# Optimization experiments

Hardware: AMD Instinct MI355X
Metric: run time of the kernel (lower is better)

The kernel has to match this reference:

```python
import jax, jax.numpy as jnp
import numpy as np

N, E, B = 60000, 360000, 64        # nodes, edges, graphs
IN_DIM, HID, L, NCLS = 256, 512, 3, 1000
EPS = 1e-5                          # BatchNorm1d eps


def setup_inputs() -> dict:
    key = jax.random.key(0)
    ks = jax.random.split(key, 10)
    s = 0.05
    x = jax.random.normal(ks[0], (N, IN_DIM), dtype=jnp.float32)
    edge_index = jax.random.randint(ks[1], (2, E), 0, N, dtype=jnp.int32)
    batch = jnp.sort(jax.random.randint(ks[2], (N,), 0, B, dtype=jnp.int32))
    W_embed = jax.random.normal(ks[3], (IN_DIM, HID), dtype=jnp.float32) * s
    # per-block params (all 3 blocks have identical shapes -> stacked on axis 0)
    W1 = jax.random.normal(ks[4], (L, 2 * HID, HID), dtype=jnp.float32) * s
    b1 = jnp.zeros((L, HID), jnp.float32)
    g1 = jnp.ones((L, HID), jnp.float32)
    be1 = jnp.zeros((L, HID), jnp.float32)
    W2 = jax.random.normal(ks[5], (L, 2 * HID, HID), dtype=jnp.float32) * s
    b2 = jnp.zeros((L, HID), jnp.float32)
    g2 = jnp.ones((L, HID), jnp.float32)
    be2 = jnp.zeros((L, HID), jnp.float32)
    W_att = jax.random.normal(ks[6], (HID, 1), dtype=jnp.float32) * s
    W_read = jax.random.normal(ks[7], (HID, NCLS), dtype=jnp.float32) * s
    return dict(x=x, edge_index=edge_index, batch=batch, W_embed=W_embed,
                W1=W1, b1=b1, g1=g1, be1=be1, W2=W2, b2=b2, g2=g2, be2=be2,
                W_att=W_att, W_read=W_read)


def _segment_mean(vals, idx, num):
    s = jax.ops.segment_sum(vals, idx, num_segments=num)
    c = jax.ops.segment_sum(jnp.ones((vals.shape[0], 1), vals.dtype), idx, num_segments=num)
    return s / jnp.maximum(c, 1.0)


def _bn(h, g, b):  # BatchNorm1d, training-mode batch statistics (biased var)
    m = h.mean(0)
    v = jnp.mean((h - m) ** 2, axis=0)
    return (h - m) * jax.lax.rsqrt(v + EPS) * g + b


def _sage(h, src, dst, W, b):
    # MySAGEConv (position=False -> message = x_j), aggr='mean', concat=True, L2 normalize
    aggr = _segment_mean(h[src], dst, h.shape[0])          # [N, d] mean of neighbor msgs
    out = jnp.concatenate([h, aggr], axis=-1) @ W + b      # [N, 2d] @ [2d, d]
    norm = jnp.linalg.norm(out, axis=-1, keepdims=True)
    return out / jnp.maximum(norm, 1e-12)                  # F.normalize(p=2)


def reference(x, edge_index, batch, W_embed, W1, b1, g1, be1,
              W2, b2, g2, be2, W_att, W_read):
    src, dst = edge_index[0], edge_index[1]
    h = x @ W_embed
    for l in range(L):  # MySAGEConvBlock, gcn_num=2, has_linear_in_block=False
        identity = h
        out = jax.nn.relu(_bn(_sage(h, src, dst, W1[l], b1[l]), g1[l], be1[l]))
        out = jax.nn.relu(_bn(_sage(out, src, dst, W2[l], b2[l]), g2[l], be2[l]))
        h = out + identity  # residual (dims match)
    # AttentionClass
    att = jax.nn.sigmoid(h @ W_att)           # [N, 1]
    hx = (att * h + h) * 0.5
    hg = _segment_mean(hx, batch, B)          # global mean pool per graph
    return hg @ W_read                        # [B, 1000] logits
```

## Files before the change

### kernel.cpp

```cpp
#include <hip/hip_runtime.h>
#include <math.h>

#define N_NODES 60000
#define N_EDGES 360000
#define N_GRAPH 64
#define HID 512
#define NCLS 1000
#define BN_EPS 1e-5f
#define NS ((size_t)N_NODES * HID)
#define NB 235
#define STRIPS 469

typedef __bf16 bf16x8 __attribute__((ext_vector_type(8)));
typedef float f32x4 __attribute__((ext_vector_type(4)));

static __device__ __forceinline__ unsigned short f2bf(float f) {
  unsigned u = __float_as_uint(f);
  unsigned r = (u + 0x7fffu + ((u >> 16) & 1u)) >> 16;
  return (unsigned short)r;
}
static __device__ __forceinline__ float bfLo(unsigned u) { return __uint_as_float(u << 16); }
static __device__ __forceinline__ float bfHi(unsigned u) { return __uint_as_float(u & 0xffff0000u); }
static __device__ __forceinline__ unsigned packbf(float a, float b) {
  return (unsigned)f2bf(a) | ((unsigned)f2bf(b) << 16);
}

__global__ void write_sentinel(float* out, float v) { out[0] = v; }

__global__ __launch_bounds__(256) void cvt_bf16(const float* __restrict__ X,
                                                unsigned short* __restrict__ Y,
                                                long n4) {
  long i = (long)blockIdx.x * 256 + threadIdx.x;
  if (i >= n4) return;
  float4 f = *(const float4*)(X + i * 4);
  uint2 o;
  o.x = packbf(f.x, f.y);
  o.y = packbf(f.z, f.w);
  *(uint2*)(Y + i * 4) = o;
}

__global__ __launch_bounds__(256) void wtrans(const float* __restrict__ W,
                                              unsigned short* __restrict__ Wt,
                                              int K, int N) {
  __shared__ float sh[32][33];
  int kt = blockIdx.x * 32, nt = blockIdx.y * 32;
  int tx = threadIdx.x & 31, ty = threadIdx.x >> 5;
#pragma unroll
  for (int i = 0; i < 4; ++i)
    sh[ty + i * 8][tx] = W[(size_t)(kt + ty + i * 8) * N + nt + tx];
  __syncthreads();
#pragma unroll
  for (int i = 0; i < 4; ++i)
    Wt[(size_t)(nt + ty + i * 8) * K + kt + tx] = f2bf(sh[tx][ty + i * 8]);
}

__global__ __launch_bounds__(256) void count_deg(const int* __restrict__ dst,
                                                 int* __restrict__ deg, int E) {
  int e = blockIdx.x * 256 + threadIdx.x;
  if (e < E) atomicAdd(&deg[dst[e]], 1);
}

__global__ __launch_bounds__(256) void make_invdeg(const int* __restrict__ deg,
                                                   float* __restrict__ inv, int n) {
  int i = blockIdx.x * 256 + threadIdx.x;
  if (i < n) inv[i] = 1.0f / fmaxf((float)deg[i], 1.0f);
}

__global__ __launch_bounds__(256) void scan_part(const int* __restrict__ deg,
                                                 int* __restrict__ bsum, int n) {
  __shared__ int sh[256];
  int i = blockIdx.x * 256 + threadIdx.x;
  sh[threadIdx.x] = (i < n) ? deg[i] : 0;
  __syncthreads();
  for (int off = 128; off; off >>= 1) {
    if (threadIdx.x < off) sh[threadIdx.x] += sh[threadIdx.x + off];
    __syncthreads();
  }
  if (threadIdx.x == 0) bsum[blockIdx.x] = sh[0];
}

__global__ __launch_bounds__(256) void scan_bsums(int* __restrict__ bsum, int nb) {
  __shared__ int sh[256];
  int t = threadIdx.x;
  int v = (t < nb) ? bsum[t] : 0;
  sh[t] = v;
  __syncthreads();
  for (int off = 1; off < 256; off <<= 1) {
    int u = (t >= off) ? sh[t - off] : 0;
    __syncthreads();
    sh[t] += u;
    __syncthreads();
  }
  if (t < nb) bsum[t] = sh[t] - v;
}

__global__ __launch_bounds__(256) void scan_final(const int* __restrict__ deg,
                                                  const int* __restrict__ bsum,
                                                  int* __restrict__ rowptr, int n) {
  __shared__ int sh[256];
  int t = threadIdx.x;
  int i = blockIdx.x * 256 + t;
  int v = (i < n) ? deg[i] : 0;
  sh[t] = v;
  __syncthreads();
  for (int off = 1; off < 256; off <<= 1) {
    int u = (t >= off) ? sh[t - off] : 0;
    __syncthreads();
    sh[t] += u;
    __syncthreads();
  }
  if (i < n) rowptr[i + 1] = bsum[blockIdx.x] + sh[t];
  if (i == 0) rowptr[0] = 0;
}

__global__ __launch_bounds__(256) void fill_csr(const int* __restrict__ src,
                                                const int* __restrict__ dst,
                                                const int* __restrict__ rowptr,
                                                int* __restrict__ fillc,
                                                int* __restrict__ esrc, int E) {
  int e = blockIdx.x * 256 + threadIdx.x;
  if (e < E) {
    int d = dst[e];
    int pos = rowptr[d] + atomicAdd(&fillc[d], 1);
    esrc[pos] = src[e];
  }
}

__global__ __launch_bounds__(256) void bcount(const int* __restrict__ batch,
                                              float* __restrict__ bcnt, int n) {
  __shared__ int h[N_GRAPH];
  if (threadIdx.x < N_GRAPH) h[threadIdx.x] = 0;
  __syncthreads();
  int i = blockIdx.x * 256 + threadIdx.x;
  if (i < n) atomicAdd(&h[batch[i]], 1);
  __syncthreads();
  if (threadIdx.x < N_GRAPH && h[threadIdx.x])
    atomicAdd(&bcnt[threadIdx.x], (float)h[threadIdx.x]);
}

#define GEMM_BODY(Xb, ldx, Wtb, ldw, bias_p, outp, KDIM)                        \
  const int wv = tid >> 6, lane = tid & 63;                                     \
  const int wm = (wv >> 1) * 64, wn = (wv & 1) * 64;                            \
  const int lm = lane & 15, quad = lane >> 4;                                   \
  const int grow = lane & 15, gseg = (lane >> 4) * 8;                           \
  f32x4 zero; zero[0] = 0.f; zero[1] = 0.f; zero[2] = 0.f; zero[3] = 0.f;       \
  f32x4 acc[4][4];                                                              \
  _Pragma("unroll") for (int i = 0; i < 4; ++i)                                 \
    _Pragma("unroll") for (int j = 0; j < 4; ++j) acc[i][j] = zero;             \
  for (int kt = 0; kt < (KDIM); kt += 32) {                                     \
    __syncthreads();                                                            \
    _Pragma("unroll") for (int r = 0; r < 2; ++r) {                             \
      int chunk = wv + r * 4;                                                   \
      int row = chunk * 16 + grow;                                              \
      const unsigned short* ga = (Xb) + (size_t)(bm + row) * (ldx) + kt + gseg; \
      const unsigned short* gb = (Wtb) + (size_t)(bn + row) * (ldw) + kt + gseg;\
      __builtin_amdgcn_global_load_lds(                                         \
          (const __attribute__((address_space(1))) unsigned int*)ga,            \
          (__attribute__((address_space(3))) unsigned int*)(As + chunk * 512),  \
          16, 0, 0);                                                            \
      __builtin_amdgcn_global_load_lds(                                         \
          (const __attribute__((address_space(1))) unsigned int*)gb,            \
          (__attribute__((address_space(3))) unsigned int*)(Bs + chunk * 512),  \
          16, 0, 0);                                                            \
    }                                                                           \
    __syncthreads();                                                            \
    bf16x8 af[4], bfr[4];                                                       \
    _Pragma("unroll") for (int i = 0; i < 4; ++i)                               \
      af[i] = *(const bf16x8*)(As + (wm / 16 + i) * 512 + lane * 8);            \
    _Pragma("unroll") for (int j = 0; j < 4; ++j)                               \
      bfr[j] = *(const bf16x8*)(Bs + (wn / 16 + j) * 512 + lane * 8);           \
    _Pragma("unroll") for (int i = 0; i < 4; ++i)                               \
      _Pragma("unroll") for (int j = 0; j < 4; ++j)                             \
        acc[i][j] = __builtin_amdgcn_mfma_f32_16x16x32_bf16(af[i], bfr[j],      \
                                                            acc[i][j], 0, 0, 0);\
  }                                                                             \
  const int qr = quad * 4;                                                      \
  const int rl = tid >> 4, seg = (tid & 15) * 8;                                \
  _Pragma("unroll") for (int p = 0; p < 2; ++p) {                               \
    __syncthreads();                                                            \
    if ((wv >> 1) == p) {                                                       \
      _Pragma("unroll") for (int j = 0; j < 4; ++j) {                           \
        int col = wn + j * 16 + lm;                                             \
        float bvv = (bias_p) ? (bias_p)[bn + col] : 0.f;                        \
        _Pragma("unroll") for (int i = 0; i < 4; ++i)                           \
          _Pragma("unroll") for (int r = 0; r < 4; ++r)                         \
            Cs[i * 16 + qr + r][col] = f2bf(acc[i][j][r] + bvv);                \
      }                                                                         \
    }                                                                           \
    __syncthreads();                                                            \
    _Pragma("unroll") for (int pass = 0; pass < 4; ++pass) {                    \
      int row = bm + p * 64 + pass * 16 + rl;                                   \
      if (row < M)                                                              \
        *(uint4*)((outp) + (size_t)row * 512 + bn + seg) =                      \
            *(const uint4*)(&Cs[pass * 16 + rl][seg]);                          \
    }                                                                           \
  }

__global__ __launch_bounds__(256) void gemm_glds(
    const unsigned short* __restrict__ Xb, int ldx, int K,
    const unsigned short* __restrict__ Wt, int ldw,
    const float* __restrict__ bias,
    unsigned short* __restrict__ outB, int M) {
  __shared__ __align__(16) unsigned short As[128 * 32];
  __shared__ __align__(16) unsigned short Bs[128 * 32];
  __shared__ __align__(16) unsigned short Cs[64][136];
  const int tid = threadIdx.x;
  const int L = blockIdx.x;
  const int xcd = L & 7, li = L >> 3;
  const int strip = xcd * 59 + (li >> 2);
  if (strip >= STRIPS) return;
  const int bm = strip * 128;
  const int bn = (li & 3) * 128;
  GEMM_BODY(Xb, ldx, Wt, ldw, bias, outB, K)
}

__global__ __launch_bounds__(256) void gemm_dual(
    const unsigned short* __restrict__ Xb, int ldx,
    const unsigned short* __restrict__ Wt,
    const float* __restrict__ biasA,
    unsigned short* __restrict__ outA, unsigned short* __restrict__ outBf,
    int M) {
  __shared__ __align__(16) unsigned short As[128 * 32];
  __shared__ __align__(16) unsigned short Bs[128 * 32];
  __shared__ __align__(16) unsigned short Cs[64][136];
  const int tid = threadIdx.x;
  const int L = blockIdx.x;
  const int xcd = L & 7, li = L >> 3;
  const int strip = xcd * 59 + (li >> 3);
  if (strip >= STRIPS) return;
  const int cb = li & 7;
  const int bm = strip * 128;
  const int bn = (cb & 3) * 128;
  const unsigned short* Wtb = Wt + (cb < 4 ? 0 : 512);
  const float* bias = (cb < 4) ? biasA : nullptr;
  unsigned short* outp = (cb < 4) ? outA : outBf;
  GEMM_BODY(Xb, ldx, Wtb, 1024, bias, outp, 512)
}

__global__ __launch_bounds__(512) void gemm_strip(
    const unsigned short* __restrict__ Xb, int ldx,
    const unsigned short* __restrict__ Wt, int ldw,
    const float* __restrict__ bias,
    unsigned short* __restrict__ outB, int M) {
  __shared__ __align__(16) unsigned short As[64][40];
  const int tid = threadIdx.x;
  const int bm = blockIdx.x * 64;
  const int wv = tid >> 6, lane = tid & 63;
  const int lm = lane & 15, quad = lane >> 4, lk = quad * 8;
  const int cb = wv * 64;
  const int arow = tid >> 3, aseg = (tid & 7) * 4;

  f32x4 zero;
  zero[0] = 0.f; zero[1] = 0.f; zero[2] = 0.f; zero[3] = 0.f;
  f32x4 acc[4][4];
#pragma unroll
  for (int i = 0; i < 4; ++i)
#pragma unroll
    for (int j = 0; j < 4; ++j) acc[i][j] = zero;

  for (int kt = 0; kt < 512; kt += 32) {
    uint2 av = make_uint2(0, 0);
    int gr = bm + arow;
    if (gr < M) av = *(const uint2*)(Xb + (size_t)gr * ldx + kt + aseg);
    bf16x8 bfr[4];
#pragma unroll
    for (int j = 0; j < 4; ++j)
      bfr[j] = *(const bf16x8*)(Wt + (size_t)(cb + j * 16 + lm) * ldw + kt + lk);
    __syncthreads();
    *(uint2*)(&As[arow][aseg]) = av;
    __syncthreads();
    bf16x8 af[4];
#pragma unroll
    for (int i = 0; i < 4; ++i) af[i] = *(const bf16x8*)(&As[i * 16 + lm][lk]);
#pragma unroll
    for (int i = 0; i < 4; ++i)
#pragma unroll
      for (int j = 0; j < 4; ++j)
        acc[i][j] = __builtin_amdgcn_mfma_f32_16x16x32_bf16(af[i], bfr[j], acc[i][j], 0, 0, 0);
  }

  const int qr = quad * 4;
#pragma unroll
  for (int j = 0; j < 4; ++j) {
    int col = cb + j * 16 + lm;
    float bvv = bias ? bias[col] : 0.f;
#pragma unroll
    for (int i = 0; i < 4; ++i) {
      int rbase = bm + i * 16 + qr;
#pragma unroll
      for (int r = 0; r < 4; ++r) {
        int row = rbase + r;
        if (row < M) outB[(size_t)row * 512 + col] = f2bf(acc[i][j][r] + bvv);
      }
    }
  }
}

__global__ __launch_bounds__(256) void aggr_norm(
    unsigned short* __restrict__ Ya, const unsigned short* __restrict__ Yb,
    const int* __restrict__ rowptr, const int* __restrict__ esrc,
    const float* __restrict__ invdeg, int M) {
  int d = blockIdx.x * 4 + (threadIdx.x >> 6);
  int lane = threadIdx.x & 63;
  if (d >= M) return;
  float acc[8] = {0.f, 0.f, 0.f, 0.f, 0.f, 0.f, 0.f, 0.f};
  int beg = rowptr[d], end = rowptr[d + 1];
  for (int e = beg; e < end; ++e) {
    int s = esrc[e];
    uint4 u = *(const uint4*)(Yb + (size_t)s * 512 + lane * 8);
    acc[0] += bfLo(u.x); acc[1] += bfHi(u.x);
    acc[2] += bfLo(u.y); acc[3] += bfHi(u.y);
    acc[4] += bfLo(u.z); acc[5] += bfHi(u.z);
    acc[6] += bfLo(u.w); acc[7] += bfHi(u.w);
  }
  float iv = invdeg[d];
  uint4 a = *(const uint4*)(Ya + (size_t)d * 512 + lane * 8);
  float r0 = bfLo(a.x) + iv * acc[0], r1 = bfHi(a.x) + iv * acc[1];
  float r2 = bfLo(a.y) + iv * acc[2], r3 = bfHi(a.y) + iv * acc[3];
  float r4 = bfLo(a.z) + iv * acc[4], r5 = bfHi(a.z) + iv * acc[5];
  float r6 = bfLo(a.w) + iv * acc[6], r7 = bfHi(a.w) + iv * acc[7];
  float ss = r0 * r0 + r1 * r1 + r2 * r2 + r3 * r3
           + r4 * r4 + r5 * r5 + r6 * r6 + r7 * r7;
#pragma unroll
  for (int o = 32; o; o >>= 1) ss += __shfl_xor(ss, o, 64);
  float inv = 1.0f / fmaxf(sqrtf(ss), 1e-12f);
  uint4 o4;
  o4.x = packbf(r0 * inv, r1 * inv);
  o4.y = packbf(r2 * inv, r3 * inv);
  o4.z = packbf(r4 * inv, r5 * inv);
  o4.w = packbf(r6 * inv, r7 * inv);
  *(uint4*)(Ya + (size_t)d * 512 + lane * 8) = o4;
}

__global__ __launch_bounds__(256) void bn_stats(const unsigned short* __restrict__ T,
                                                int M, float* __restrict__ sums) {
  const int t = threadIdx.x;
  int r0 = blockIdx.x * 128;
  int rend = min(r0 + 128, M);
  float s0 = 0.f, q0 = 0.f, s1 = 0.f, q1 = 0.f;
  for (int r = r0; r < rend; ++r) {
    float a = __uint_as_float((unsigned)T[(size_t)r * 512 + t] << 16);
    float b = __uint_as_float((unsigned)T[(size_t)r * 512 + t + 256] << 16);
    s0 += a; q0 += a * a; s1 += b; q1 += b * b;
  }
  atomicAdd(&sums[t], s0);
  atomicAdd(&sums[t + 256], s1);
  atomicAdd(&sums[512 + t], q0);
  atomicAdd(&sums[512 + t + 256], q1);
}

__global__ __launch_bounds__(256) void bn_apply(const unsigned short* __restrict__ U,
                                                unsigned short* __restrict__ H,
                                                const float* __restrict__ sums,
                                                const float* __restrict__ g,
                                                const float* __restrict__ be,
                                                int M, int residual) {
  size_t i2 = (size_t)blockIdx.x * 256 + threadIdx.x;
  if (i2 >= NS / 2) return;
  int c = ((int)(i2 & 255)) * 2;
  float invM = 1.0f / (float)M;
  float m0 = sums[c] * invM, m1 = sums[c + 1] * invM;
  float v0 = sums[512 + c] * invM - m0 * m0;
  float v1 = sums[512 + c + 1] * invM - m1 * m1;
  float k0 = rsqrtf(v0 + BN_EPS) * g[c], k1 = rsqrtf(v1 + BN_EPS) * g[c + 1];
  unsigned u = ((const unsigned*)U)[i2];
  float x0 = fmaxf((bfLo(u) - m0) * k0 + be[c], 0.f);
  float x1 = fmaxf((bfHi(u) - m1) * k1 + be[c + 1], 0.f);
  if (residual) {
    unsigned hv = ((const unsigned*)H)[i2];
    x0 += bfLo(hv);
    x1 += bfHi(hv);
  }
  ((unsigned*)H)[i2] = packbf(x0, x1);
}

#define NPB 64
__global__ __launch_bounds__(256) void att_pool2(const unsigned short* __restrict__ H,
                                                 const int* __restrict__ batch,
                                                 const float* __restrict__ Watt,
                                                 float* __restrict__ hg, int M) {
  __shared__ float fsh[NPB];
  __shared__ int bsh[NPB];
  const int tid = threadIdx.x;
  const int base = blockIdx.x * NPB;
  if (tid < NPB) bsh[tid] = (base + tid < M) ? batch[base + tid] : -1;
  const int wv = tid >> 6, lane = tid & 63;
  float4 wa0 = *(const float4*)(Watt + lane * 8);
  float4 wa1 = *(const float4*)(Watt + lane * 8 + 4);
  __syncthreads();
  for (int i = wv; i < NPB; i += 4) {
    int node = base + i;
    float dot = 0.f;
    if (node < M) {
      uint4 u = *(const uint4*)(H + (size_t)node * 512 + lane * 8);
      dot = bfLo(u.x) * wa0.x + bfHi(u.x) * wa0.y
          + bfLo(u.y) * wa0.z + bfHi(u.y) * wa0.w
          + bfLo(u.z) * wa1.x + bfHi(u.z) * wa1.y
          + bfLo(u.w) * wa1.z + bfHi(u.w) * wa1.w;
    }
#pragma unroll
    for (int o = 32; o; o >>= 1) dot += __shfl_xor(dot, o, 64);
    if (lane == 0) fsh[i] = 0.5f * (1.0f + 1.0f / (1.0f + expf(-dot)));
  }
  __syncthreads();
  float a0 = 0.f, a1 = 0.f;
  int cur = bsh[0];
  for (int i = 0; i < NPB; ++i) {
    int node = base + i;
    if (node >= M) break;
    int b = bsh[i];
    if (b != cur) {
      atomicAdd(&hg[(size_t)cur * 512 + tid * 2], a0);
      atomicAdd(&hg[(size_t)cur * 512 + tid * 2 + 1], a1);
      a0 = a1 = 0.f;
      cur = b;
    }
    unsigned u = *(const unsigned*)(H + (size_t)node * 512 + tid * 2);
    float f = fsh[i];
    a0 += bfLo(u) * f;
    a1 += bfHi(u) * f;
  }
  if (cur >= 0) {
    atomicAdd(&hg[(size_t)cur * 512 + tid * 2], a0);
    atomicAdd(&hg[(size_t)cur * 512 + tid * 2 + 1], a1);
  }
}

__global__ __launch_bounds__(256) void readout(const float* __restrict__ hg,
                                               const float* __restrict__ bcnt,
                                               const float* __restrict__ Wr,
                                               float* __restrict__ out) {
  __shared__ float sh[HID];
  int g = blockIdx.x;
  int n = blockIdx.y * 256 + threadIdx.x;
  float inv = 1.0f / fmaxf(bcnt[g], 1.0f);
  for (int k = threadIdx.x; k < HID; k += 256) sh[k] = hg[(size_t)g * HID + k] * inv;
  __syncthreads();
  if (n < NCLS) {
    float acc = 0.f;
    for (int k = 0; k < HID; ++k) acc += sh[k] * Wr[(size_t)k * NCLS + n];
    out[(size_t)g * NCLS + n] = acc;
  }
}

extern "C" void kernel_launch(void* const* d_in, const int* in_sizes, int n_in,
                              void* d_out, int out_size, void* d_ws, size_t ws_size,
                              hipStream_t stream) {
  const float* x       = (const float*)d_in[0];
  const int*   ei      = (const int*)d_in[1];
  const int*   batch   = (const int*)d_in[2];
  const float* W_embed = (const float*)d_in[3];
  const float* W1      = (const float*)d_in[4];
  const float* b1      = (const float*)d_in[5];
  const float* g1      = (const float*)d_in[6];
  const float* be1     = (const float*)d_in[7];
  const float* W2      = (const float*)d_in[8];
  const float* b2      = (const float*)d_in[9];
  const float* g2      = (const float*)d_in[10];
  const float* be2     = (const float*)d_in[11];
  const float* Watt    = (const float*)d_in[12];
  const float* Wread   = (const float*)d_in[13];
  float* out = (float*)d_out;

  const int* srcIdx = ei;
  const int* dstIdx = ei + N_EDGES;

  char* p = (char*)d_ws;
  unsigned short* B0 = (unsigned short*)p; p += NS * 2;
  unsigned short* B1 = (unsigned short*)p; p += NS * 2;
  unsigned short* B2 = (unsigned short*)p; p += NS * 2;
  unsigned short* WtE = (unsigned short*)p; p += (size_t)512 * 256 * 2;
  unsigned short* Wt1 = (unsigned short*)p; p += (size_t)3 * 512 * 1024 * 2;
  unsigned short* Wt2 = (unsigned short*)p; p += (size_t)3 * 512 * 1024 * 2;
  float* hg     = (float*)p; p += (size_t)N_GRAPH * HID * 4;
  float* sums   = (float*)p; p += 1024 * 4;
  float* invdeg = (float*)p; p += (size_t)N_NODES * 4;
  float* bcnt   = (float*)p; p += 256;
  int* deg      = (int*)p;   p += (size_t)N_NODES * 4;
  int* fillc    = (int*)p;   p += (size_t)N_NODES * 4;
  int* esrc     = (int*)p;   p += (size_t)N_EDGES * 4;
  int* rowptr   = (int*)p;   p += (size_t)(N_NODES + 1) * 4;
  int* bsum     = (int*)p;   p += (size_t)NB * 4;
  size_t need = (size_t)(p - (char*)d_ws);
  if (ws_size < need) {
    write_sentinel<<<1, 1, 0, stream>>>(out, (float)need);
    return;
  }

  wtrans<<<dim3(8, 16), 256, 0, stream>>>(W_embed, WtE, 256, 512);
  for (int l = 0; l < 3; ++l) {
    wtrans<<<dim3(32, 16), 256, 0, stream>>>(W1 + (size_t)l * 1024 * 512,
                                             Wt1 + (size_t)l * 512 * 1024, 1024, 512);
    wtrans<<<dim3(32, 16), 256, 0, stream>>>(W2 + (size_t)l * 1024 * 512,
                                             Wt2 + (size_t)l * 512 * 1024, 1024, 512);
  }

  hipMemsetAsync(deg, 0, N_NODES * sizeof(int), stream);
  hipMemsetAsync(fillc, 0, N_NODES * sizeof(int), stream);
  count_deg<<<(N_EDGES + 255) / 256, 256, 0, stream>>>(dstIdx, deg, N_EDGES);
  make_invdeg<<<(N_NODES + 255) / 256, 256, 0, stream>>>(deg, invdeg, N_NODES);
  scan_part<<<NB, 256, 0, stream>>>(deg, bsum, N_NODES);
  scan_bsums<<<1, 256, 0, stream>>>(bsum, NB);
  scan_final<<<NB, 256, 0, stream>>>(deg, bsum, rowptr, N_NODES);
  fill_csr<<<(N_EDGES + 255) / 256, 256, 0, stream>>>(srcIdx, dstIdx, rowptr, fillc,
                                                      esrc, N_EDGES);

  const int g1grid = 8 * 59 * 4;
  const int g2grid = 8 * 59 * 8;
  const int sgrid  = (N_NODES + 63) / 64;
  const int ngrid  = (N_NODES + 3) / 4;
  const int bgrid  = (N_NODES + 127) / 128;
  const int egrid  = (int)((NS / 2 + 255) / 256);

  cvt_bf16<<<(int)(((size_t)N_NODES * 64 + 255) / 256), 256, 0, stream>>>(
      x, B1, (long)N_NODES * 64);
  gemm_glds<<<g1grid, 256, 0, stream>>>(B1, 256, 256, WtE, 256, nullptr, B0, N_NODES);

  for (int l = 0; l < 3; ++l) {
    const unsigned short* Wt1l = Wt1 + (size_t)l * 512 * 1024;
    const unsigned short* Wt2l = Wt2 + (size_t)l * 512 * 1024;
    gemm_dual<<<g2grid, 256, 0, stream>>>(B0, 512, Wt1l, b1 + l * 512, B1, B2, N_NODES);
    aggr_norm<<<ngrid, 256, 0, stream>>>(B1, B2, rowptr, esrc, invdeg, N_NODES);
    hipMemsetAsync(sums, 0, 1024 * sizeof(float), stream);
    bn_stats<<<bgrid, 256, 0, stream>>>(B1, N_NODES, sums);
    bn_apply<<<egrid, 256, 0, stream>>>(B1, B1, sums, g1 + l * 512,
                                        be1 + l * 512, N_NODES, 0);
    gemm_glds<<<g1grid, 256, 0, stream>>>(B1, 512, 512, Wt2l + 512, 1024,
                                          nullptr, B2, N_NODES);
    gemm_strip<<<sgrid, 512, 0, stream>>>(B1, 512, Wt2l, 1024,
                                          b2 + l * 512, B1, N_NODES);
    aggr_norm<<<ngrid, 256, 0, stream>>>(B1, B2, rowptr, esrc, invdeg, N_NODES);
    hipMemsetAsync(sums, 0, 1024 * sizeof(float), stream);
    bn_stats<<<bgrid, 256, 0, stream>>>(B1, N_NODES, sums);
    bn_apply<<<egrid, 256, 0, stream>>>(B1, B0, sums, g2 + l * 512,
                                        be2 + l * 512, N_NODES, 1);
  }

  hipMemsetAsync(hg, 0, (size_t)N_GRAPH * HID * sizeof(float), stream);
  hipMemsetAsync(bcnt, 0, N_GRAPH * sizeof(float), stream);
  bcount<<<NB, 256, 0, stream>>>(batch, bcnt, N_NODES);
  att_pool2<<<(N_NODES + NPB - 1) / NPB, 256, 0, stream>>>(B0, batch, Watt, hg, N_NODES);
  readout<<<dim3(N_GRAPH, 4), 256, 0, stream>>>(hg, bcnt, Wread, out);
}
```

Before: 2.084 ms.

## Use dual GEMM for second conv, vectorize BN apply, batch weight transposes

When the workspace has room for an extra activation buffer, the second SAGE conv in each block runs as one dual-output GEMM in place of the separate gemm_glds plus gemm_strip launches. bn_apply now processes eight bf16 values per thread with 16-byte loads and stores. bn_stats uses 32 rows per block to raise parallelism, at the cost of more atomics. The per-layer weight transposes are batched into launches indexed by grid z. The dual-GEMM path depends on the caller providing a larger workspace and falls back to the old path otherwise.

```diff
diff --git a/kernel.cpp b/kernel.cpp
--- a/kernel.cpp
+++ b/kernel.cpp
@@ -41,8 +41,11 @@
 
 __global__ __launch_bounds__(256) void wtrans(const float* __restrict__ W,
                                               unsigned short* __restrict__ Wt,
-                                              int K, int N) {
+                                              int K, int N,
+                                              size_t strideW, size_t strideWt) {
   __shared__ float sh[32][33];
+  W += (size_t)blockIdx.z * strideW;
+  Wt += (size_t)blockIdx.z * strideWt;
   int kt = blockIdx.x * 32, nt = blockIdx.y * 32;
   int tx = threadIdx.x & 31, ty = threadIdx.x >> 5;
 #pragma unroll
@@ -335,8 +338,8 @@
 __global__ __launch_bounds__(256) void bn_stats(const unsigned short* __restrict__ T,
                                                 int M, float* __restrict__ sums) {
   const int t = threadIdx.x;
-  int r0 = blockIdx.x * 128;
-  int rend = min(r0 + 128, M);
+  int r0 = blockIdx.x * 32;
+  int rend = min(r0 + 32, M);
   float s0 = 0.f, q0 = 0.f, s1 = 0.f, q1 = 0.f;
   for (int r = r0; r < rend; ++r) {
     float a = __uint_as_float((unsigned)T[(size_t)r * 512 + t] << 16);
@@ -355,23 +358,30 @@
                                                 const float* __restrict__ g,
                                                 const float* __restrict__ be,
                                                 int M, int residual) {
-  size_t i2 = (size_t)blockIdx.x * 256 + threadIdx.x;
-  if (i2 >= NS / 2) return;
-  int c = ((int)(i2 & 255)) * 2;
+  size_t i4 = (size_t)blockIdx.x * 256 + threadIdx.x;
+  if (i4 >= NS / 8) return;
+  int c = (int)((i4 * 8) & 511);
   float invM = 1.0f / (float)M;
-  float m0 = sums[c] * invM, m1 = sums[c + 1] * invM;
-  float v0 = sums[512 + c] * invM - m0 * m0;
-  float v1 = sums[512 + c + 1] * invM - m1 * m1;
-  float k0 = rsqrtf(v0 + BN_EPS) * g[c], k1 = rsqrtf(v1 + BN_EPS) * g[c + 1];
-  unsigned u = ((const unsigned*)U)[i2];
-  float x0 = fmaxf((bfLo(u) - m0) * k0 + be[c], 0.f);
-  float x1 = fmaxf((bfHi(u) - m1) * k1 + be[c + 1], 0.f);
-  if (residual) {
-    unsigned hv = ((const unsigned*)H)[i2];
-    x0 += bfLo(hv);
-    x1 += bfHi(hv);
-  }
-  ((unsigned*)H)[i2] = packbf(x0, x1);
+  uint4 u4 = ((const uint4*)U)[i4];
+  uint4 h4;
+  if (residual) h4 = ((const uint4*)H)[i4];
+  unsigned uin[4] = {u4.x, u4.y, u4.z, u4.w};
+  unsigned hin[4] = {h4.x, h4.y, h4.z, h4.w};
+  unsigned outv[4];
+#pragma unroll
+  for (int k = 0; k < 4; ++k) {
+    int c0 = c + k * 2;
+    float m0 = sums[c0] * invM, m1 = sums[c0 + 1] * invM;
+    float v0 = sums[512 + c0] * invM - m0 * m0;
+    float v1 = sums[512 + c0 + 1] * invM - m1 * m1;
+    float k0 = rsqrtf(v0 + BN_EPS) * g[c0], k1 = rsqrtf(v1 + BN_EPS) * g[c0 + 1];
+    float x0 = fmaxf((bfLo(uin[k]) - m0) * k0 + be[c0], 0.f);
+    float x1 = fmaxf((bfHi(uin[k]) - m1) * k1 + be[c0 + 1], 0.f);
+    if (residual) { x0 += bfLo(hin[k]); x1 += bfHi(hin[k]); }
+    outv[k] = packbf(x0, x1);
+  }
+  uint4 o4 = make_uint4(outv[0], outv[1], outv[2], outv[3]);
+  ((uint4*)H)[i4] = o4;
 }
 
 #define NPB 64
@@ -486,14 +496,14 @@
     write_sentinel<<<1, 1, 0, stream>>>(out, (float)need);
     return;
   }
-
-  wtrans<<<dim3(8, 16), 256, 0, stream>>>(W_embed, WtE, 256, 512);
-  for (int l = 0; l < 3; ++l) {
-    wtrans<<<dim3(32, 16), 256, 0, stream>>>(W1 + (size_t)l * 1024 * 512,
-                                             Wt1 + (size_t)l * 512 * 1024, 1024, 512);
-    wtrans<<<dim3(32, 16), 256, 0, stream>>>(W2 + (size_t)l * 1024 * 512,
-                                             Wt2 + (size_t)l * 512 * 1024, 1024, 512);
-  }
+  unsigned short* B3 = nullptr;
+  if (ws_size >= need + NS * 2) B3 = (unsigned short*)((char*)d_ws + need);
+
+  wtrans<<<dim3(8, 16, 1), 256, 0, stream>>>(W_embed, WtE, 256, 512, 0, 0);
+  wtrans<<<dim3(32, 16, 3), 256, 0, stream>>>(W1, Wt1, 1024, 512,
+                                              (size_t)1024 * 512, (size_t)512 * 1024);
+  wtrans<<<dim3(32, 16, 3), 256, 0, stream>>>(W2, Wt2, 1024, 512,
+                                              (size_t)1024 * 512, (size_t)512 * 1024);
 
   hipMemsetAsync(deg, 0, N_NODES * sizeof(int), stream);
   hipMemsetAsync(fillc, 0, N_NODES * sizeof(int), stream);
@@ -509,8 +519,8 @@
   const int g2grid = 8 * 59 * 8;
   const int sgrid  = (N_NODES + 63) / 64;
   const int ngrid  = (N_NODES + 3) / 4;
-  const int bgrid  = (N_NODES + 127) / 128;
-  const int egrid  = (int)((NS / 2 + 255) / 256);
+  const int bgrid  = (N_NODES + 31) / 32;
+  const int egrid  = (int)((NS / 8 + 255) / 256);
 
   cvt_bf16<<<(int)(((size_t)N_NODES * 64 + 255) / 256), 256, 0, stream>>>(
       x, B1, (long)N_NODES * 64);
@@ -525,14 +535,20 @@
     bn_stats<<<bgrid, 256, 0, stream>>>(B1, N_NODES, sums);
     bn_apply<<<egrid, 256, 0, stream>>>(B1, B1, sums, g1 + l * 512,
                                         be1 + l * 512, N_NODES, 0);
-    gemm_glds<<<g1grid, 256, 0, stream>>>(B1, 512, 512, Wt2l + 512, 1024,
-                                          nullptr, B2, N_NODES);
-    gemm_strip<<<sgrid, 512, 0, stream>>>(B1, 512, Wt2l, 1024,
-                                          b2 + l * 512, B1, N_NODES);
-    aggr_norm<<<ngrid, 256, 0, stream>>>(B1, B2, rowptr, esrc, invdeg, N_NODES);
+    unsigned short* Ya2 = B3 ? B3 : B1;
+    if (B3) {
+      gemm_dual<<<g2grid, 256, 0, stream>>>(B1, 512, Wt2l, b2 + l * 512, B3, B2,
+                                            N_NODES);
+    } else {
+      gemm_glds<<<g1grid, 256, 0, stream>>>(B1, 512, 512, Wt2l + 512, 1024,
+                                            nullptr, B2, N_NODES);
+      gemm_strip<<<sgrid, 512, 0, stream>>>(B1, 512, Wt2l, 1024,
+                                            b2 + l * 512, B1, N_NODES);
+    }
+    aggr_norm<<<ngrid, 256, 0, stream>>>(Ya2, B2, rowptr, esrc, invdeg, N_NODES);
     hipMemsetAsync(sums, 0, 1024 * sizeof(float), stream);
-    bn_stats<<<bgrid, 256, 0, stream>>>(B1, N_NODES, sums);
-    bn_apply<<<egrid, 256, 0, stream>>>(B1, B0, sums, g2 + l * 512,
+    bn_stats<<<bgrid, 256, 0, stream>>>(Ya2, N_NODES, sums);
+    bn_apply<<<egrid, 256, 0, stream>>>(Ya2, B0, sums, g2 + l * 512,
                                         be2 + l * 512, N_NODES, 1);
   }
 
```

Result: faster. 1.968 ms (-5.5%).
